# Performance work log

Measured on AMD Instinct MI355X. Metric: run time of the kernel, lower is better.

Reference implementation:

```python
import jax, jax.numpy as jnp
import numpy as np
from jax import lax

T_DATA = 20000
E_NO = 2000
I_NO = 500
SUB_NO = 16
SYN_B = 3
HID = 256
T_SYN = 200
T_ENC = 80


def _causal_conv(x, kern):
    # x: [T, S] per-subunit drive; kern: [S, K] causal kernels (index = lag)
    S, K = kern.shape
    lhs = jnp.pad(x.T, ((0, 0), (K - 1, 0)))[None]        # [1, S, T+K-1]
    rhs = kern[:, ::-1][:, None, :]                        # flip then correlate == torch conv1d path
    out = lax.conv_general_dilated(lhs, rhs, (1,), 'VALID', feature_group_count=S)
    return out[0].T                                        # [T, S]


def setup_inputs() -> dict:
    key = jax.random.key(0)
    ks = jax.random.split(key, 16)
    V_in = jax.random.normal(ks[0], (T_DATA,), jnp.float32) * 5.0 - 69.0
    S_e = jax.random.bernoulli(ks[1], 0.02, (T_DATA, E_NO)).astype(jnp.float32)
    S_i = jax.random.bernoulli(ks[2], 0.02, (T_DATA, I_NO)).astype(jnp.float32)
    # synapse -> subunit one-hot assignment matrices [sub_no, n_syn]
    C_syn_e = jax.nn.one_hot(jax.random.randint(ks[3], (E_NO,), 0, SUB_NO), SUB_NO, dtype=jnp.float32).T
    C_syn_i = jax.nn.one_hot(jax.random.randint(ks[4], (I_NO,), 0, SUB_NO), SUB_NO, dtype=jnp.float32).T
    # parameters, initialized exactly as in __init__
    K_syn = jnp.stack([jnp.full((SUB_NO, SYN_B), 0.04),
                       jnp.full((SUB_NO, SYN_B), -0.02),
                       jnp.full((SUB_NO, SYN_B), 0.02)], axis=-1)          # [sub, B, 3]
    tau_syn = jnp.tile((jnp.arange(SYN_B, dtype=jnp.float32) + 1.6)[:, None], (1, 3))  # [B, 3]
    delta_syn = jnp.full((SUB_NO, 2), 2.0, jnp.float32)
    enc_bias = jnp.zeros((SUB_NO - 1,), jnp.float32)
    W_in = 2 * T_ENC - 1

    def lin(k, fan_out, fan_in):
        kw, kb = jax.random.split(k)
        s = 1.0 / np.sqrt(fan_in)
        return (jax.random.uniform(kw, (fan_out, fan_in), jnp.float32, -s, s),
                jax.random.uniform(kb, (fan_out,), jnp.float32, -s, s))

    W1, b1 = lin(ks[5], HID, W_in)
    W2, b2 = lin(ks[6], HID, HID)
    W3, b3 = lin(ks[7], HID, HID)
    W4, b4 = lin(ks[8], SUB_NO - 1, HID)
    a1 = jnp.float32(0.25)
    a2 = jnp.float32(0.25)
    a3 = jnp.float32(0.25)
    return dict(V_in=V_in, S_e=S_e, S_i=S_i, C_syn_e=C_syn_e, C_syn_i=C_syn_i,
                K_syn=K_syn, tau_syn=tau_syn, delta_syn=delta_syn, enc_bias=enc_bias,
                W1=W1, b1=b1, a1=a1, W2=W2, b2=b2, a2=a2, W3=W3, b3=b3, a3=a3,
                W4=W4, b4=b4)


def reference(V_in, S_e, S_i, C_syn_e, C_syn_i, K_syn, tau_syn, delta_syn, enc_bias,
              W1, b1, a1, W2, b2, a2, W3, b3, a3, W4, b4):
    T = V_in.shape[0]
    # ---- spike_convolve, fully vectorized over (subunit, basis) ----
    t = jnp.arange(T_SYN, dtype=V_in.dtype)                 # [T_syn]
    d = jnp.exp(delta_syn)                                   # [sub, 2]
    te = jnp.maximum(t[None, :] - d[:, 0:1], 0.0)            # [sub, T_syn]
    ti = jnp.maximum(t[None, :] - d[:, 1:2], 0.0)
    tau = jnp.exp(tau_syn)                                   # [B, 3]
    tte = te[:, None, :] / tau[None, :, 0, None]             # [sub, B, T_syn]
    tti = ti[:, None, :] / tau[None, :, 1, None]
    ker_e = jnp.einsum('sbt,sb->st', tte * jnp.exp(-tte), K_syn[:, :, 0])
    ker_i = jnp.einsum('sbt,sb->st', tti * jnp.exp(-tti), K_syn[:, :, 1])
    in_e = S_e @ C_syn_e.T                                   # [T, sub]
    in_i = S_i @ C_syn_i.T
    S_conv = _causal_conv(in_e, ker_e) + _causal_conv(in_i, ker_i)   # [T, sub]
    # ---- encode: batched sliding-window MLP (replaces per-timestep loop) ----
    W = 2 * T_ENC - 1
    Vpad = jnp.zeros((T + W,), V_in.dtype).at[T_ENC - 1:T_ENC - 1 + T].set(V_in)
    idx = jnp.arange(T)[:, None] + jnp.arange(W)[None, :]    # [T, W]
    win = Vpad[idx]                                          # [T, W]
    prelu = lambda x, a: jnp.where(x >= 0, x, a * x)
    h = prelu(win @ W1.T + b1, a1)
    h = prelu(h @ W2.T + b2, a2)
    h = prelu(h @ W3.T + b3, a3)
    nn_out = h @ W4.T + b4                                   # [T, sub-1]
    return jax.nn.sigmoid(nn_out + S_conv[:, 1:] + enc_bias)
```

## Files before the change

kernel.cpp:

```cpp
#include <hip/hip_runtime.h>
#include <cstdint>
#include <cstddef>

#define T_DATA 20000
#define E_NO 2000
#define I_NO 500
#define SUB_NO 16
#define HID 256
#define T_SYN 200
#define T_ENC 80
#define W_IN 159

typedef __attribute__((ext_vector_type(8))) __bf16 bf16x8;
typedef __attribute__((ext_vector_type(8))) short short8;
typedef __attribute__((ext_vector_type(4))) float floatx4;
typedef __attribute__((ext_vector_type(4))) unsigned int uint4v;
typedef __attribute__((ext_vector_type(2))) unsigned int uint2v;

__device__ __forceinline__ float bf2f(unsigned short u) {
    union { unsigned int i; float f; } v; v.i = ((unsigned int)u) << 16; return v.f;
}
__device__ __forceinline__ unsigned short f2bf(float f) {
    union { float f; unsigned int i; } v; v.f = f;
    unsigned int r = v.i + 0x7FFFu + ((v.i >> 16) & 1u);
    return (unsigned short)(r >> 16);
}
__device__ __forceinline__ float inload(const void* p, int i, int isbf) {
    return isbf ? bf2f(((const unsigned short*)p)[i]) : ((const float*)p)[i];
}

__device__ __forceinline__ int detect_bf(const void* Se, int* sfl) {
    if (threadIdx.x == 0) *sfl = 0;
    __syncthreads();
    const unsigned int* w = (const unsigned int*)Se;
    int la = 0;
    #pragma unroll
    for (int i = 0; i < 4; i++)
        la |= (w[i * 256 + threadIdx.x] & 0xFFFFu) ? 1 : 0;
    if (la) atomicOr(sfl, 1);
    __syncthreads();
    return *sfl;
}

#define OFF_KERE   16u
#define OFF_KERI   12816u
#define OFF_SHE    25616u
#define OFF_SHI    33616u
#define OFF_W1H    35616u
#define OFF_W1L    117536u
#define OFF_W2H    199456u
#define OFF_W2L    330528u
#define OFF_W3H    461600u
#define OFF_W3L    592672u
#define OFF_W4H    723744u
#define OFF_W4L    731936u
#define OFF_INE    740128u
#define OFF_INI    1060128u

__global__ void k_tables(const void* Se, const void* Ksyn, const void* tau_syn, const void* dly,
                         const void* Ce, const void* Ci,
                         float* ker_e, float* ker_i, unsigned char* sh_e, unsigned char* sh_i) {
    __shared__ int sfl;
    int f = detect_bf(Se, &sfl);
    int id = blockIdx.x * 256 + threadIdx.x;
    if (id < 6400) {
        int c = id < 3200 ? 0 : 1;
        int q = id - c * 3200;
        int s = q / 200, j = q - s * 200;
        float d = expf(inload(dly, s * 2 + c, f));
        float tt = fmaxf((float)j - d, 0.0f);
        float acc = 0.f;
        #pragma unroll
        for (int b = 0; b < 3; b++) {
            float tau = expf(inload(tau_syn, b * 3 + c, f));
            float x = tt / tau;
            acc += x * expf(-x) * inload(Ksyn, (s * 3 + b) * 3 + c, f);
        }
        (c == 0 ? ker_e : ker_i)[s * 200 + j] = acc;
    } else if (id < 8400) {
        int e = id - 6400;
        int a = 0;
        for (int s = 0; s < 16; s++) if (inload(Ce, s * E_NO + e, f) > 0.5f) a = s;
        sh_e[e] = (unsigned char)(a * 8);
    } else if (id < 8900) {
        int e = id - 8400;
        int a = 0;
        for (int s = 0; s < 16; s++) if (inload(Ci, s * I_NO + e, f) > 0.5f) a = s;
        sh_i[e] = (unsigned char)(a * 8);
    }
}

__device__ __forceinline__ void acc_slot(unsigned int b, unsigned int sh,
                                         unsigned long long& lo, unsigned long long& hi) {
    unsigned int up = sh >> 6;
    unsigned int s6 = sh & 63;
    lo += (unsigned long long)(b & (up ^ 1u)) << s6;
    hi += (unsigned long long)(b & up) << s6;
}

__global__ void __launch_bounds__(256) k_spikes(const void* Se, const void* Si,
                         const unsigned char* sh_e, const unsigned char* sh_i,
                         const void* W1, const void* W2, const void* W3, const void* W4,
                         unsigned char* in_e, unsigned char* in_i,
                         unsigned short* W1h, unsigned short* W1l,
                         unsigned short* W2h, unsigned short* W2l,
                         unsigned short* W3h, unsigned short* W3l,
                         unsigned short* W4h, unsigned short* W4l) {
    __shared__ int sfl;
    __shared__ __align__(8) unsigned char she[E_NO];
    __shared__ __align__(8) unsigned char shi[I_NO];
    for (int i = threadIdx.x; i < E_NO / 4; i += 256)
        ((unsigned int*)she)[i] = ((const unsigned int*)sh_e)[i];
    for (int i = threadIdx.x; i < I_NO / 4; i += 256)
        ((unsigned int*)shi)[i] = ((const unsigned int*)sh_i)[i];
    int f = detect_bf(Se, &sfl);
    int lane = threadIdx.x & 63;
    int wave = threadIdx.x >> 6;
    int t = blockIdx.x * 4 + wave;
    unsigned long long e0 = 0, e1 = 0, i0 = 0, i1 = 0;
    if (f) {
        const uint4v* re = (const uint4v*)((const unsigned short*)Se + (size_t)t * E_NO);
        #pragma unroll
        for (int it = 0; it < 4; it++) {
            int c = it * 64 + lane;
            if (c < 250) {
                uint4v v = re[c];
                unsigned long long q = *(const unsigned long long*)&she[c * 8];
                #pragma unroll
                for (int w = 0; w < 4; w++) {
                    unsigned int x = v[w];
                    acc_slot((x >> 7) & 1u,  (unsigned int)(q >> (16 * w)) & 0xFFu, e0, e1);
                    acc_slot((x >> 23) & 1u, (unsigned int)(q >> (16 * w + 8)) & 0xFFu, e0, e1);
                }
            }
        }
        const uint2v* ri = (const uint2v*)((const unsigned short*)Si + (size_t)t * I_NO);
        #pragma unroll
        for (int it = 0; it < 2; it++) {
            int c = it * 64 + lane;
            if (c < 125) {
                uint2v v = ri[c];
                unsigned int q = *(const unsigned int*)&shi[c * 4];
                #pragma unroll
                for (int w = 0; w < 2; w++) {
                    unsigned int x = v[w];
                    acc_slot((x >> 7) & 1u,  (q >> (16 * w)) & 0xFFu, i0, i1);
                    acc_slot((x >> 23) & 1u, (q >> (16 * w + 8)) & 0xFFu, i0, i1);
                }
            }
        }
    } else {
        const uint4v* re = (const uint4v*)((const float*)Se + (size_t)t * E_NO);
        #pragma unroll
        for (int it = 0; it < 8; it++) {
            int c = it * 64 + lane;
            if (c < 500) {
                uint4v v = re[c];
                unsigned int q = *(const unsigned int*)&she[c * 4];
                #pragma unroll
                for (int w = 0; w < 4; w++)
                    acc_slot((v[w] >> 23) & 1u, (q >> (8 * w)) & 0xFFu, e0, e1);
            }
        }
        const uint2v* ri = (const uint2v*)((const float*)Si + (size_t)t * I_NO);
        #pragma unroll
        for (int it = 0; it < 4; it++) {
            int c = it * 64 + lane;
            if (c < 250) {
                uint2v v = ri[c];
                unsigned int q = *(const unsigned short*)&shi[c * 2];
                #pragma unroll
                for (int w = 0; w < 2; w++)
                    acc_slot((v[w] >> 23) & 1u, (q >> (8 * w)) & 0xFFu, i0, i1);
            }
        }
    }
    for (int off = 32; off; off >>= 1) {
        e0 += __shfl_xor(e0, off);
        e1 += __shfl_xor(e1, off);
        i0 += __shfl_xor(i0, off);
        i1 += __shfl_xor(i1, off);
    }
    if (lane < 16) {
        unsigned long long a = (lane < 8) ? e0 : e1;
        in_e[(size_t)t * 16 + lane] = (unsigned char)((a >> ((lane & 7) * 8)) & 0xFF);
    } else if (lane < 32) {
        int s = lane - 16;
        unsigned long long a = (s < 8) ? i0 : i1;
        in_i[(size_t)t * 16 + s] = (unsigned char)((a >> ((s & 7) * 8)) & 0xFF);
    }
    if (blockIdx.x < 688) {
        int q = blockIdx.x * 256 + threadIdx.x;
        if (q < 40960) {
            int j = q & 7, l = (q >> 3) & 63, r = q >> 9;
            int ks = r % 5, tile = r / 5;
            int n = tile * 16 + (l & 15);
            int k = ks * 32 + (l >> 4) * 8 + j;
            float v = (k < W_IN) ? inload(W1, n * W_IN + k, f) : 0.f;
            unsigned short hi = f2bf(v);
            W1h[q] = hi;
            W1l[q] = f2bf(v - bf2f(hi));
        } else if (q < 106496) {
            int p = q - 40960;
            int j = p & 7, l = (p >> 3) & 63, r = p >> 9;
            int ks = r & 7, tile = r >> 3;
            int n = tile * 16 + (l & 15);
            int k = ks * 32 + (l >> 4) * 8 + j;
            float v = inload(W2, n * 256 + k, f);
            unsigned short hi = f2bf(v);
            W2h[p] = hi;
            W2l[p] = f2bf(v - bf2f(hi));
        } else if (q < 172032) {
            int p = q - 106496;
            int j = p & 7, l = (p >> 3) & 63, r = p >> 9;
            int ks = r & 7, tile = r >> 3;
            int n = tile * 16 + (l & 15);
            int k = ks * 32 + (l >> 4) * 8 + j;
            float v = inload(W3, n * 256 + k, f);
            unsigned short hi = f2bf(v);
            W3h[p] = hi;
            W3l[p] = f2bf(v - bf2f(hi));
        } else {
            int p = q - 172032;
            int j = p & 7, l = (p >> 3) & 63, ks = p >> 9;
            int lm = l & 15, quad = l >> 4;
            float v = 0.f;
            if (lm < 15) v = inload(W4, lm * 256 + ks * 32 + quad * 8 + j, f);
            unsigned short hi = f2bf(v);
            W4h[p] = hi;
            W4l[p] = f2bf(v - bf2f(hi));
        }
    }
}

template<bool BF>
__device__ __forceinline__ void mlp_body(
    const void* V,
    const unsigned short* W1h, const unsigned short* W1l, const void* b1, const void* a1p,
    const unsigned short* W2h, const unsigned short* W2l, const void* b2, const void* a2p,
    const unsigned short* W3h, const unsigned short* W3l, const void* b3, const void* a3p,
    const unsigned short* W4h, const unsigned short* W4l, const void* b4,
    const void* encb, const float* Sc, void* out,
    unsigned short* Ahi, unsigned short* Alo,
    const bf16x8 (&Bh1)[5][4])
{
    int tid = threadIdx.x;
    int lane = tid & 63, wave = tid >> 6;
    int lm = lane & 15, quad = lane >> 4;
    int t0 = blockIdx.x * 64;

    auto ld = [&](const void* p, int i) -> float {
        return BF ? bf2f(((const unsigned short*)p)[i]) : ((const float*)p)[i];
    };
    auto boff1 = [&](int ks, int nt) { return (size_t)((((wave * 4 + nt) * 5 + ks) * 64 + lane) << 3); };
    auto boff  = [&](int ks, int nt) { return (size_t)((((wave * 4 + nt) * 8 + ks) * 64 + lane) << 3); };

    for (int idx = tid; idx < 64 * 160; idx += 256) {
        int m = idx / 160, k = idx - m * 160;
        int tg = t0 + m + k - (T_ENC - 1);
        float v = 0.f;
        if (k < W_IN && tg >= 0 && tg < T_DATA) v = ld(V, tg);
        unsigned short hi = f2bf(v);
        int col = (((k >> 3) ^ (m & 31)) << 3) | (k & 7);
        Ahi[m * 256 + col] = hi;
        if (!BF) Alo[m * 256 + col] = f2bf(v - bf2f(hi));
    }
    __syncthreads();

    floatx4 acc[4][4];
    auto aoff = [&](int mt, int ks) {
        int arow = mt * 16 + lm;
        return arow * 256 + ((((ks << 2) | quad) ^ (arow & 31)) << 3);
    };

    auto epi = [&](const void* bias, float alpha) {
        __syncthreads();
        #pragma unroll
        for (int mt = 0; mt < 4; mt++) {
            #pragma unroll
            for (int nt = 0; nt < 4; nt++) {
                int cn = wave * 64 + nt * 16 + lm;
                float bb = ld(bias, cn);
                #pragma unroll
                for (int j = 0; j < 4; j++) {
                    int row = mt * 16 + quad * 4 + j;
                    float h = acc[mt][nt][j] + bb;
                    h = (h >= 0.f) ? h : alpha * h;
                    unsigned short hi = f2bf(h);
                    int col = (((cn >> 3) ^ (row & 31)) << 3) | (cn & 7);
                    Ahi[row * 256 + col] = hi;
                    if (!BF) Alo[row * 256 + col] = f2bf(h - bf2f(hi));
                }
            }
        }
        __syncthreads();
    };

    floatx4 z = {0.f, 0.f, 0.f, 0.f};
    {
        #pragma unroll
        for (int mt = 0; mt < 4; mt++)
            #pragma unroll
            for (int nt = 0; nt < 4; nt++) acc[mt][nt] = z;
        if (BF) {
            #pragma unroll
            for (int ks = 0; ks < 5; ks++) {
                bf16x8 a[4];
                #pragma unroll
                for (int mt = 0; mt < 4; mt++) a[mt] = *(const bf16x8*)&Ahi[aoff(mt, ks)];
                #pragma unroll
                for (int nt = 0; nt < 4; nt++)
                    #pragma unroll
                    for (int mt = 0; mt < 4; mt++)
                        acc[mt][nt] = __builtin_amdgcn_mfma_f32_16x16x32_bf16(a[mt], Bh1[ks][nt], acc[mt][nt], 0, 0, 0);
            }
        } else {
            #pragma unroll
            for (int ks = 0; ks < 5; ks++) {
                bf16x8 ah[4], al[4];
                #pragma unroll
                for (int mt = 0; mt < 4; mt++) {
                    ah[mt] = *(const bf16x8*)&Ahi[aoff(mt, ks)];
                    al[mt] = *(const bf16x8*)&Alo[aoff(mt, ks)];
                }
                #pragma unroll
                for (int nt = 0; nt < 4; nt++) {
                    bf16x8 bh = Bh1[ks][nt];
                    bf16x8 bl = *(const bf16x8*)(W1l + boff1(ks, nt));
                    #pragma unroll
                    for (int mt = 0; mt < 4; mt++) {
                        acc[mt][nt] = __builtin_amdgcn_mfma_f32_16x16x32_bf16(ah[mt], bh, acc[mt][nt], 0, 0, 0);
                        acc[mt][nt] = __builtin_amdgcn_mfma_f32_16x16x32_bf16(al[mt], bh, acc[mt][nt], 0, 0, 0);
                        acc[mt][nt] = __builtin_amdgcn_mfma_f32_16x16x32_bf16(ah[mt], bl, acc[mt][nt], 0, 0, 0);
                    }
                }
            }
        }
        epi(b1, ld(a1p, 0));
    }
    const unsigned short* Whs[2] = {W2h, W3h};
    const unsigned short* Wls[2] = {W2l, W3l};
    const void* bs[2] = {b2, b3};
    const void* as_[2] = {a2p, a3p};
    for (int l = 0; l < 2; l++) {
        #pragma unroll
        for (int mt = 0; mt < 4; mt++)
            #pragma unroll
            for (int nt = 0; nt < 4; nt++) acc[mt][nt] = z;
        const unsigned short* Wh = Whs[l];
        const unsigned short* Wl = Wls[l];
        if (BF) {
            bf16x8 Bh[8][4];
            #pragma unroll
            for (int ks = 0; ks < 8; ks++)
                #pragma unroll
                for (int nt = 0; nt < 4; nt++)
                    Bh[ks][nt] = *(const bf16x8*)(Wh + boff(ks, nt));
            #pragma unroll
            for (int ks = 0; ks < 8; ks++) {
                bf16x8 a[4];
                #pragma unroll
                for (int mt = 0; mt < 4; mt++) a[mt] = *(const bf16x8*)&Ahi[aoff(mt, ks)];
                #pragma unroll
                for (int nt = 0; nt < 4; nt++)
                    #pragma unroll
                    for (int mt = 0; mt < 4; mt++)
                        acc[mt][nt] = __builtin_amdgcn_mfma_f32_16x16x32_bf16(a[mt], Bh[ks][nt], acc[mt][nt], 0, 0, 0);
            }
        } else {
            #pragma unroll
            for (int ks = 0; ks < 8; ks++) {
                bf16x8 ah[4], al[4];
                #pragma unroll
                for (int mt = 0; mt < 4; mt++) {
                    ah[mt] = *(const bf16x8*)&Ahi[aoff(mt, ks)];
                    al[mt] = *(const bf16x8*)&Alo[aoff(mt, ks)];
                }
                #pragma unroll
                for (int nt = 0; nt < 4; nt++) {
                    bf16x8 bh = *(const bf16x8*)(Wh + boff(ks, nt));
                    bf16x8 bl = *(const bf16x8*)(Wl + boff(ks, nt));
                    #pragma unroll
                    for (int mt = 0; mt < 4; mt++) {
                        acc[mt][nt] = __builtin_amdgcn_mfma_f32_16x16x32_bf16(ah[mt], bh, acc[mt][nt], 0, 0, 0);
                        acc[mt][nt] = __builtin_amdgcn_mfma_f32_16x16x32_bf16(al[mt], bh, acc[mt][nt], 0, 0, 0);
                        acc[mt][nt] = __builtin_amdgcn_mfma_f32_16x16x32_bf16(ah[mt], bl, acc[mt][nt], 0, 0, 0);
                    }
                }
            }
        }
        epi(bs[l], ld(as_[l], 0));
    }
    {
        int mt = wave;
        floatx4 a4 = z;
        #pragma unroll
        for (int ks = 0; ks < 8; ks++) {
            bf16x8 ah = *(const bf16x8*)&Ahi[aoff(mt, ks)];
            bf16x8 bh = *(const bf16x8*)(W4h + (size_t)((ks * 64 + lane) << 3));
            a4 = __builtin_amdgcn_mfma_f32_16x16x32_bf16(ah, bh, a4, 0, 0, 0);
            if (!BF) {
                bf16x8 al = *(const bf16x8*)&Alo[aoff(mt, ks)];
                bf16x8 bl = *(const bf16x8*)(W4l + (size_t)((ks * 64 + lane) << 3));
                a4 = __builtin_amdgcn_mfma_f32_16x16x32_bf16(al, bh, a4, 0, 0, 0);
                a4 = __builtin_amdgcn_mfma_f32_16x16x32_bf16(ah, bl, a4, 0, 0, 0);
            }
        }
        if (lm < 15) {
            float bb = ld(b4, lm) + ld(encb, lm);
            #pragma unroll
            for (int j = 0; j < 4; j++) {
                int row = mt * 16 + quad * 4 + j;
                int t = t0 + row;
                if (t < T_DATA) {
                    float x = a4[j] + bb + Sc[row * 16 + lm + 1];
                    x = fminf(fmaxf(x, -40.f), 40.f);
                    float sg = 1.f / (1.f + expf(-x));
                    if (BF) ((unsigned short*)out)[(size_t)t * 15 + lm] = f2bf(sg);
                    else    ((float*)out)[(size_t)t * 15 + lm] = sg;
                }
            }
        }
    }
}

__global__ void __launch_bounds__(256, 2) k_convmlp(
    const void* Se, const void* V,
    const unsigned char* in_e, const unsigned char* in_i,
    const float* ker_e, const float* ker_i,
    const unsigned short* W1h, const unsigned short* W1l, const void* b1, const void* a1p,
    const unsigned short* W2h, const unsigned short* W2l, const void* b2, const void* a2p,
    const unsigned short* W3h, const unsigned short* W3l, const void* b3, const void* a3p,
    const unsigned short* W4h, const unsigned short* W4l, const void* b4,
    const void* encb, void* out) {
    __shared__ __align__(16) unsigned char smem[65536];
    __shared__ __align__(16) float Sc[64 * 16];
    __shared__ int sfl;

    float* se = (float*)smem;
    float* si = se + 263 * 17;
    float* ke = si + 263 * 17;
    float* ki = ke + 16 * 201;

    int lane = threadIdx.x & 63, wave = threadIdx.x >> 6;

    bf16x8 Bh1[5][4];
    #pragma unroll
    for (int ks = 0; ks < 5; ks++)
        #pragma unroll
        for (int nt = 0; nt < 4; nt++)
            Bh1[ks][nt] = *(const bf16x8*)(W1h + (size_t)((((wave * 4 + nt) * 5 + ks) * 64 + lane) << 3));

    int t0 = blockIdx.x * 64;
    for (int idx = threadIdx.x; idx < 263 * 4; idx += 256) {
        int r = idx >> 2, wi = idx & 3;
        int t = t0 - 199 + r;
        unsigned int ve = 0, vi = 0;
        if (t >= 0 && t < T_DATA) {
            ve = ((const unsigned int*)in_e)[t * 4 + wi];
            vi = ((const unsigned int*)in_i)[t * 4 + wi];
        }
        #pragma unroll
        for (int b = 0; b < 4; b++) {
            se[r * 17 + wi * 4 + b] = (float)((ve >> (8 * b)) & 0xFF);
            si[r * 17 + wi * 4 + b] = (float)((vi >> (8 * b)) & 0xFF);
        }
    }
    for (int idx = threadIdx.x; idx < 3200; idx += 256) {
        int s2 = idx / 200, j = idx - s2 * 200;
        ke[s2 * 201 + j] = ker_e[idx];
        ki[s2 * 201 + j] = ker_i[idx];
    }
    int f = detect_bf(Se, &sfl);

    {
        int s = threadIdx.x & 15, g4 = (threadIdx.x >> 4) * 4;
        float a0 = 0.f, a1 = 0.f, a2 = 0.f, a3 = 0.f;
        float w0 = se[(g4 + 199) * 17 + s], w1 = se[(g4 + 200) * 17 + s];
        float w2 = se[(g4 + 201) * 17 + s], w3 = se[(g4 + 202) * 17 + s];
        float x0 = si[(g4 + 199) * 17 + s], x1 = si[(g4 + 200) * 17 + s];
        float x2 = si[(g4 + 201) * 17 + s], x3 = si[(g4 + 202) * 17 + s];
        #pragma unroll 4
        for (int j = 0; j < 200; j++) {
            float kej = ke[s * 201 + j];
            float kij = ki[s * 201 + j];
            a0 += w0 * kej + x0 * kij;
            a1 += w1 * kej + x1 * kij;
            a2 += w2 * kej + x2 * kij;
            a3 += w3 * kej + x3 * kij;
            int lr = g4 + 198 - j; lr = lr < 0 ? 0 : lr;
            float nw = se[lr * 17 + s], nx = si[lr * 17 + s];
            w3 = w2; w2 = w1; w1 = w0; w0 = nw;
            x3 = x2; x2 = x1; x1 = x0; x0 = nx;
        }
        Sc[(g4 + 0) * 16 + s] = a0;
        Sc[(g4 + 1) * 16 + s] = a1;
        Sc[(g4 + 2) * 16 + s] = a2;
        Sc[(g4 + 3) * 16 + s] = a3;
    }
    __syncthreads();

    unsigned short* Ahi = (unsigned short*)smem;
    unsigned short* Alo = Ahi + 64 * 256;
    if (f)
        mlp_body<true>(V, W1h, W1l, b1, a1p, W2h, W2l, b2, a2p, W3h, W3l, b3, a3p,
                       W4h, W4l, b4, encb, Sc, out, Ahi, Alo, Bh1);
    else
        mlp_body<false>(V, W1h, W1l, b1, a1p, W2h, W2l, b2, a2p, W3h, W3l, b3, a3p,
                        W4h, W4l, b4, encb, Sc, out, Ahi, Alo, Bh1);
}

extern "C" void kernel_launch(void* const* d_in, const int* in_sizes, int n_in,
                              void* d_out, int out_size, void* d_ws, size_t ws_size,
                              hipStream_t stream) {
    const void* V    = d_in[0];
    const void* Se   = d_in[1];
    const void* Si   = d_in[2];
    const void* Ce   = d_in[3];
    const void* Ci   = d_in[4];
    const void* Ksyn = d_in[5];
    const void* tau  = d_in[6];
    const void* dly  = d_in[7];
    const void* encb = d_in[8];
    const void* W1   = d_in[9];
    const void* b1   = d_in[10];
    const void* a1   = d_in[11];
    const void* W2   = d_in[12];
    const void* b2   = d_in[13];
    const void* a2   = d_in[14];
    const void* W3   = d_in[15];
    const void* b3   = d_in[16];
    const void* a3   = d_in[17];
    const void* W4   = d_in[18];
    const void* b4   = d_in[19];

    char* w = (char*)d_ws;
    float* ker_e = (float*)(w + OFF_KERE);
    float* ker_i = (float*)(w + OFF_KERI);
    unsigned char* sh_e = (unsigned char*)(w + OFF_SHE);
    unsigned char* sh_i = (unsigned char*)(w + OFF_SHI);
    unsigned short* W1h = (unsigned short*)(w + OFF_W1H);
    unsigned short* W1l = (unsigned short*)(w + OFF_W1L);
    unsigned short* W2h = (unsigned short*)(w + OFF_W2H);
    unsigned short* W2l = (unsigned short*)(w + OFF_W2L);
    unsigned short* W3h = (unsigned short*)(w + OFF_W3H);
    unsigned short* W3l = (unsigned short*)(w + OFF_W3L);
    unsigned short* W4h = (unsigned short*)(w + OFF_W4H);
    unsigned short* W4l = (unsigned short*)(w + OFF_W4L);
    unsigned char* in_e = (unsigned char*)(w + OFF_INE);
    unsigned char* in_i = (unsigned char*)(w + OFF_INI);

    k_tables<<<35, 256, 0, stream>>>(Se, Ksyn, tau, dly, Ce, Ci,
                                     ker_e, ker_i, sh_e, sh_i);
    k_spikes<<<5000, 256, 0, stream>>>(Se, Si, sh_e, sh_i, W1, W2, W3, W4,
                                       in_e, in_i,
                                       W1h, W1l, W2h, W2l, W3h, W3l, W4h, W4l);
    k_convmlp<<<313, 256, 0, stream>>>(Se, V, in_e, in_i, ker_e, ker_i,
                                       W1h, W1l, b1, a1, W2h, W2l, b2, a2,
                                       W3h, W3l, b3, a3, W4h, W4l, b4,
                                       encb, d_out);
}
```

Before: 355.4 us.

## Use 512-thread blocks in conv+MLP kernel, split N tiles across 8 waves

Doubles the block size of the fused conv/MLP kernel to 512 threads. Each wave now covers two N tiles instead of four, and the first half of the threads runs the causal convolution while the second half builds the sliding-window input tile. The spike and kernel tables in shared memory are stored in bf16/padded form, and the fp32 low-part activations move to a global workspace. The aim is more waves per block to hide latency and to overlap conv with input staging. In exchange, low-part accesses on the fp32 path now go to global memory, and the final layer uses only half of the waves.

```diff
diff --git a/kernel.cpp b/kernel.cpp
--- a/kernel.cpp
+++ b/kernel.cpp
@@ -29,14 +29,15 @@
     return isbf ? bf2f(((const unsigned short*)p)[i]) : ((const float*)p)[i];
 }
 
+template<int BLK>
 __device__ __forceinline__ int detect_bf(const void* Se, int* sfl) {
     if (threadIdx.x == 0) *sfl = 0;
     __syncthreads();
     const unsigned int* w = (const unsigned int*)Se;
     int la = 0;
     #pragma unroll
-    for (int i = 0; i < 4; i++)
-        la |= (w[i * 256 + threadIdx.x] & 0xFFFFu) ? 1 : 0;
+    for (int i = 0; i < 1024 / BLK; i++)
+        la |= (w[i * BLK + threadIdx.x] & 0xFFFFu) ? 1 : 0;
     if (la) atomicOr(sfl, 1);
     __syncthreads();
     return *sfl;
@@ -56,12 +57,13 @@
 #define OFF_W4L    731936u
 #define OFF_INE    740128u
 #define OFF_INI    1060128u
+#define OFF_ALO    1380128u
 
 __global__ void k_tables(const void* Se, const void* Ksyn, const void* tau_syn, const void* dly,
                          const void* Ce, const void* Ci,
                          float* ker_e, float* ker_i, unsigned char* sh_e, unsigned char* sh_i) {
     __shared__ int sfl;
-    int f = detect_bf(Se, &sfl);
+    int f = detect_bf<256>(Se, &sfl);
     int id = blockIdx.x * 256 + threadIdx.x;
     if (id < 6400) {
         int c = id < 3200 ? 0 : 1;
@@ -113,7 +115,7 @@
         ((unsigned int*)she)[i] = ((const unsigned int*)sh_e)[i];
     for (int i = threadIdx.x; i < I_NO / 4; i += 256)
         ((unsigned int*)shi)[i] = ((const unsigned int*)sh_i)[i];
-    int f = detect_bf(Se, &sfl);
+    int f = detect_bf<256>(Se, &sfl);
     int lane = threadIdx.x & 63;
     int wave = threadIdx.x >> 6;
     int t = blockIdx.x * 4 + wave;
@@ -235,14 +237,13 @@
 
 template<bool BF>
 __device__ __forceinline__ void mlp_body(
-    const void* V,
-    const unsigned short* W1h, const unsigned short* W1l, const void* b1, const void* a1p,
+    const unsigned short* W1l, const void* b1, const void* a1p,
     const unsigned short* W2h, const unsigned short* W2l, const void* b2, const void* a2p,
     const unsigned short* W3h, const unsigned short* W3l, const void* b3, const void* a3p,
     const unsigned short* W4h, const unsigned short* W4l, const void* b4,
     const void* encb, const float* Sc, void* out,
-    unsigned short* Ahi, unsigned short* Alo,
-    const bf16x8 (&Bh1)[5][4])
+    unsigned short* Ahi, unsigned short* AloG,
+    const bf16x8 (&Bh1)[5][2])
 {
     int tid = threadIdx.x;
     int lane = tid & 63, wave = tid >> 6;
@@ -252,86 +253,74 @@
     auto ld = [&](const void* p, int i) -> float {
         return BF ? bf2f(((const unsigned short*)p)[i]) : ((const float*)p)[i];
     };
-    auto boff1 = [&](int ks, int nt) { return (size_t)((((wave * 4 + nt) * 5 + ks) * 64 + lane) << 3); };
-    auto boff  = [&](int ks, int nt) { return (size_t)((((wave * 4 + nt) * 8 + ks) * 64 + lane) << 3); };
-
-    for (int idx = tid; idx < 64 * 160; idx += 256) {
-        int m = idx / 160, k = idx - m * 160;
-        int tg = t0 + m + k - (T_ENC - 1);
-        float v = 0.f;
-        if (k < W_IN && tg >= 0 && tg < T_DATA) v = ld(V, tg);
-        unsigned short hi = f2bf(v);
-        int col = (((k >> 3) ^ (m & 31)) << 3) | (k & 7);
-        Ahi[m * 256 + col] = hi;
-        if (!BF) Alo[m * 256 + col] = f2bf(v - bf2f(hi));
-    }
-    __syncthreads();
-
-    floatx4 acc[4][4];
+    auto boff1 = [&](int ks, int ntl) {
+        int tile = wave * 2 + ntl;
+        return (size_t)(((tile * 5 + ks) * 64 + lane) << 3);
+    };
+    auto boff = [&](int ks, int ntl) {
+        int tile = wave * 2 + ntl;
+        return (size_t)(((tile * 8 + ks) * 64 + lane) << 3);
+    };
     auto aoff = [&](int mt, int ks) {
         int arow = mt * 16 + lm;
         return arow * 256 + ((((ks << 2) | quad) ^ (arow & 31)) << 3);
     };
 
+    floatx4 z = {0.f, 0.f, 0.f, 0.f};
+    floatx4 acc[4][2];
+
     auto epi = [&](const void* bias, float alpha) {
         __syncthreads();
         #pragma unroll
         for (int mt = 0; mt < 4; mt++) {
             #pragma unroll
-            for (int nt = 0; nt < 4; nt++) {
-                int cn = wave * 64 + nt * 16 + lm;
+            for (int ntl = 0; ntl < 2; ntl++) {
+                int cn = (wave * 2 + ntl) * 16 + lm;
                 float bb = ld(bias, cn);
                 #pragma unroll
                 for (int j = 0; j < 4; j++) {
                     int row = mt * 16 + quad * 4 + j;
-                    float h = acc[mt][nt][j] + bb;
+                    float h = acc[mt][ntl][j] + bb;
                     h = (h >= 0.f) ? h : alpha * h;
                     unsigned short hi = f2bf(h);
                     int col = (((cn >> 3) ^ (row & 31)) << 3) | (cn & 7);
                     Ahi[row * 256 + col] = hi;
-                    if (!BF) Alo[row * 256 + col] = f2bf(h - bf2f(hi));
+                    if (!BF) AloG[row * 256 + col] = f2bf(h - bf2f(hi));
                 }
             }
         }
         __syncthreads();
     };
 
-    floatx4 z = {0.f, 0.f, 0.f, 0.f};
     {
         #pragma unroll
         for (int mt = 0; mt < 4; mt++)
             #pragma unroll
-            for (int nt = 0; nt < 4; nt++) acc[mt][nt] = z;
-        if (BF) {
-            #pragma unroll
-            for (int ks = 0; ks < 5; ks++) {
-                bf16x8 a[4];
-                #pragma unroll
-                for (int mt = 0; mt < 4; mt++) a[mt] = *(const bf16x8*)&Ahi[aoff(mt, ks)];
-                #pragma unroll
-                for (int nt = 0; nt < 4; nt++)
+            for (int ntl = 0; ntl < 2; ntl++) acc[mt][ntl] = z;
+        #pragma unroll
+        for (int ks = 0; ks < 5; ks++) {
+            bf16x8 ah[4];
+            #pragma unroll
+            for (int mt = 0; mt < 4; mt++) ah[mt] = *(const bf16x8*)&Ahi[aoff(mt, ks)];
+            if (BF) {
+                #pragma unroll
+                for (int ntl = 0; ntl < 2; ntl++)
                     #pragma unroll
                     for (int mt = 0; mt < 4; mt++)
-                        acc[mt][nt] = __builtin_amdgcn_mfma_f32_16x16x32_bf16(a[mt], Bh1[ks][nt], acc[mt][nt], 0, 0, 0);
-            }
-        } else {
-            #pragma unroll
-            for (int ks = 0; ks < 5; ks++) {
-                bf16x8 ah[4], al[4];
-                #pragma unroll
-                for (int mt = 0; mt < 4; mt++) {
-                    ah[mt] = *(const bf16x8*)&Ahi[aoff(mt, ks)];
-                    al[mt] = *(const bf16x8*)&Alo[aoff(mt, ks)];
-                }
-                #pragma unroll
-                for (int nt = 0; nt < 4; nt++) {
-                    bf16x8 bh = Bh1[ks][nt];
-                    bf16x8 bl = *(const bf16x8*)(W1l + boff1(ks, nt));
+                        acc[mt][ntl] = __builtin_amdgcn_mfma_f32_16x16x32_bf16(ah[mt], Bh1[ks][ntl], acc[mt][ntl], 0, 0, 0);
+            } else {
+                bf16x8 al[4];
+                #pragma unroll
+                for (int mt = 0; mt < 4; mt++) al[mt] = *(const bf16x8*)(AloG + aoff(mt, ks));
+                #pragma unroll
+                for (int ntl = 0; ntl < 2; ntl++) {
+                    bf16x8 bh = Bh1[ks][ntl];
+                    bf16x8 bl = *(const bf16x8*)(W1l + boff1(ks, ntl));
                     #pragma unroll
                     for (int mt = 0; mt < 4; mt++) {
-                        acc[mt][nt] = __builtin_amdgcn_mfma_f32_16x16x32_bf16(ah[mt], bh, acc[mt][nt], 0, 0, 0);
-                        acc[mt][nt] = __builtin_amdgcn_mfma_f32_16x16x32_bf16(al[mt], bh, acc[mt][nt], 0, 0, 0);
-                        acc[mt][nt] = __builtin_amdgcn_mfma_f32_16x16x32_bf16(ah[mt], bl, acc[mt][nt], 0, 0, 0);
+                        acc[mt][ntl] = __builtin_amdgcn_mfma_f32_16x16x32_bf16(ah[mt], bh, acc[mt][ntl], 0, 0, 0);
+                        acc[mt][ntl] = __builtin_amdgcn_mfma_f32_16x16x32_bf16(al[mt], bh, acc[mt][ntl], 0, 0, 0);
+                        acc[mt][ntl] = __builtin_amdgcn_mfma_f32_16x16x32_bf16(ah[mt], bl, acc[mt][ntl], 0, 0, 0);
                     }
                 }
             }
@@ -346,52 +335,49 @@
         #pragma unroll
         for (int mt = 0; mt < 4; mt++)
             #pragma unroll
-            for (int nt = 0; nt < 4; nt++) acc[mt][nt] = z;
+            for (int ntl = 0; ntl < 2; ntl++) acc[mt][ntl] = z;
         const unsigned short* Wh = Whs[l];
         const unsigned short* Wl = Wls[l];
-        if (BF) {
-            bf16x8 Bh[8][4];
-            #pragma unroll
-            for (int ks = 0; ks < 8; ks++)
-                #pragma unroll
-                for (int nt = 0; nt < 4; nt++)
-                    Bh[ks][nt] = *(const bf16x8*)(Wh + boff(ks, nt));
-            #pragma unroll
-            for (int ks = 0; ks < 8; ks++) {
-                bf16x8 a[4];
-                #pragma unroll
-                for (int mt = 0; mt < 4; mt++) a[mt] = *(const bf16x8*)&Ahi[aoff(mt, ks)];
-                #pragma unroll
-                for (int nt = 0; nt < 4; nt++)
+        #pragma unroll
+        for (int half = 0; half < 2; half++) {
+            bf16x8 Bh[4][2];
+            #pragma unroll
+            for (int c = 0; c < 4; c++)
+                #pragma unroll
+                for (int ntl = 0; ntl < 2; ntl++)
+                    Bh[c][ntl] = *(const bf16x8*)(Wh + boff(half * 4 + c, ntl));
+            #pragma unroll
+            for (int c = 0; c < 4; c++) {
+                int ks = half * 4 + c;
+                bf16x8 ah[4];
+                #pragma unroll
+                for (int mt = 0; mt < 4; mt++) ah[mt] = *(const bf16x8*)&Ahi[aoff(mt, ks)];
+                if (BF) {
                     #pragma unroll
-                    for (int mt = 0; mt < 4; mt++)
-                        acc[mt][nt] = __builtin_amdgcn_mfma_f32_16x16x32_bf16(a[mt], Bh[ks][nt], acc[mt][nt], 0, 0, 0);
-            }
-        } else {
-            #pragma unroll
-            for (int ks = 0; ks < 8; ks++) {
-                bf16x8 ah[4], al[4];
-                #pragma unroll
-                for (int mt = 0; mt < 4; mt++) {
-                    ah[mt] = *(const bf16x8*)&Ahi[aoff(mt, ks)];
-                    al[mt] = *(const bf16x8*)&Alo[aoff(mt, ks)];
-                }
-                #pragma unroll
-                for (int nt = 0; nt < 4; nt++) {
-                    bf16x8 bh = *(const bf16x8*)(Wh + boff(ks, nt));
-                    bf16x8 bl = *(const bf16x8*)(Wl + boff(ks, nt));
+                    for (int ntl = 0; ntl < 2; ntl++)
+                        #pragma unroll
+                        for (int mt = 0; mt < 4; mt++)
+                            acc[mt][ntl] = __builtin_amdgcn_mfma_f32_16x16x32_bf16(ah[mt], Bh[c][ntl], acc[mt][ntl], 0, 0, 0);
+                } else {
+                    bf16x8 al[4];
                     #pragma unroll
-                    for (int mt = 0; mt < 4; mt++) {
-                        acc[mt][nt] = __builtin_amdgcn_mfma_f32_16x16x32_bf16(ah[mt], bh, acc[mt][nt], 0, 0, 0);
-                        acc[mt][nt] = __builtin_amdgcn_mfma_f32_16x16x32_bf16(al[mt], bh, acc[mt][nt], 0, 0, 0);
-                        acc[mt][nt] = __builtin_amdgcn_mfma_f32_16x16x32_bf16(ah[mt], bl, acc[mt][nt], 0, 0, 0);
+                    for (int mt = 0; mt < 4; mt++) al[mt] = *(const bf16x8*)(AloG + aoff(mt, ks));
+                    #pragma unroll
+                    for (int ntl = 0; ntl < 2; ntl++) {
+                        bf16x8 bl = *(const bf16x8*)(Wl + boff(ks, ntl));
+                        #pragma unroll
+                        for (int mt = 0; mt < 4; mt++) {
+                            acc[mt][ntl] = __builtin_amdgcn_mfma_f32_16x16x32_bf16(ah[mt], Bh[c][ntl], acc[mt][ntl], 0, 0, 0);
+                            acc[mt][ntl] = __builtin_amdgcn_mfma_f32_16x16x32_bf16(al[mt], Bh[c][ntl], acc[mt][ntl], 0, 0, 0);
+                            acc[mt][ntl] = __builtin_amdgcn_mfma_f32_16x16x32_bf16(ah[mt], bl, acc[mt][ntl], 0, 0, 0);
+                        }
                     }
                 }
             }
         }
         epi(bs[l], ld(as_[l], 0));
     }
-    {
+    if (wave < 4) {
         int mt = wave;
         floatx4 a4 = z;
         #pragma unroll
@@ -400,7 +386,7 @@
             bf16x8 bh = *(const bf16x8*)(W4h + (size_t)((ks * 64 + lane) << 3));
             a4 = __builtin_amdgcn_mfma_f32_16x16x32_bf16(ah, bh, a4, 0, 0, 0);
             if (!BF) {
-                bf16x8 al = *(const bf16x8*)&Alo[aoff(mt, ks)];
+                bf16x8 al = *(const bf16x8*)(AloG + aoff(mt, ks));
                 bf16x8 bl = *(const bf16x8*)(W4l + (size_t)((ks * 64 + lane) << 3));
                 a4 = __builtin_amdgcn_mfma_f32_16x16x32_bf16(al, bh, a4, 0, 0, 0);
                 a4 = __builtin_amdgcn_mfma_f32_16x16x32_bf16(ah, bl, a4, 0, 0, 0);
@@ -424,7 +410,7 @@
     }
 }
 
-__global__ void __launch_bounds__(256, 2) k_convmlp(
+__global__ void __launch_bounds__(512, 4) k_convmlp(
     const void* Se, const void* V,
     const unsigned char* in_e, const unsigned char* in_i,
     const float* ker_e, const float* ker_i,
@@ -432,27 +418,28 @@
     const unsigned short* W2h, const unsigned short* W2l, const void* b2, const void* a2p,
     const unsigned short* W3h, const unsigned short* W3l, const void* b3, const void* a3p,
     const unsigned short* W4h, const unsigned short* W4l, const void* b4,
-    const void* encb, void* out) {
-    __shared__ __align__(16) unsigned char smem[65536];
+    const void* encb, unsigned short* AloBase, void* out) {
+    __shared__ __align__(16) unsigned short se16[263 * 17];
+    __shared__ __align__(16) unsigned short si16[263 * 17];
+    __shared__ __align__(16) float kef[16 * 204];
+    __shared__ __align__(16) float kif[16 * 204];
+    __shared__ __align__(16) unsigned short Ahi[64 * 256];
     __shared__ __align__(16) float Sc[64 * 16];
     __shared__ int sfl;
 
-    float* se = (float*)smem;
-    float* si = se + 263 * 17;
-    float* ke = si + 263 * 17;
-    float* ki = ke + 16 * 201;
-
-    int lane = threadIdx.x & 63, wave = threadIdx.x >> 6;
-
-    bf16x8 Bh1[5][4];
+    int tid = threadIdx.x;
+    int lane = tid & 63, wave = tid >> 6;
+    int t0 = blockIdx.x * 64;
+    unsigned short* AloG = AloBase + (size_t)blockIdx.x * 64 * 256;
+
+    bf16x8 Bh1[5][2];
     #pragma unroll
     for (int ks = 0; ks < 5; ks++)
         #pragma unroll
-        for (int nt = 0; nt < 4; nt++)
-            Bh1[ks][nt] = *(const bf16x8*)(W1h + (size_t)((((wave * 4 + nt) * 5 + ks) * 64 + lane) << 3));
-
-    int t0 = blockIdx.x * 64;
-    for (int idx = threadIdx.x; idx < 263 * 4; idx += 256) {
+        for (int ntl = 0; ntl < 2; ntl++)
+            Bh1[ks][ntl] = *(const bf16x8*)(W1h + (size_t)((((wave * 2 + ntl) * 5 + ks) * 64 + lane) << 3));
+
+    for (int idx = tid; idx < 263 * 4; idx += 512) {
         int r = idx >> 2, wi = idx & 3;
         int t = t0 - 199 + r;
         unsigned int ve = 0, vi = 0;
@@ -462,52 +449,64 @@
         }
         #pragma unroll
         for (int b = 0; b < 4; b++) {
-            se[r * 17 + wi * 4 + b] = (float)((ve >> (8 * b)) & 0xFF);
-            si[r * 17 + wi * 4 + b] = (float)((vi >> (8 * b)) & 0xFF);
-        }
-    }
-    for (int idx = threadIdx.x; idx < 3200; idx += 256) {
+            se16[r * 17 + wi * 4 + b] = f2bf((float)((ve >> (8 * b)) & 0xFF));
+            si16[r * 17 + wi * 4 + b] = f2bf((float)((vi >> (8 * b)) & 0xFF));
+        }
+    }
+    for (int idx = tid; idx < 3200; idx += 512) {
         int s2 = idx / 200, j = idx - s2 * 200;
-        ke[s2 * 201 + j] = ker_e[idx];
-        ki[s2 * 201 + j] = ker_i[idx];
-    }
-    int f = detect_bf(Se, &sfl);
-
-    {
-        int s = threadIdx.x & 15, g4 = (threadIdx.x >> 4) * 4;
+        kef[s2 * 204 + j] = ker_e[idx];
+        kif[s2 * 204 + j] = ker_i[idx];
+    }
+    int f = detect_bf<512>(Se, &sfl);
+
+    if (tid < 256) {
+        int s = tid & 15, g4 = (tid >> 4) * 4;
         float a0 = 0.f, a1 = 0.f, a2 = 0.f, a3 = 0.f;
-        float w0 = se[(g4 + 199) * 17 + s], w1 = se[(g4 + 200) * 17 + s];
-        float w2 = se[(g4 + 201) * 17 + s], w3 = se[(g4 + 202) * 17 + s];
-        float x0 = si[(g4 + 199) * 17 + s], x1 = si[(g4 + 200) * 17 + s];
-        float x2 = si[(g4 + 201) * 17 + s], x3 = si[(g4 + 202) * 17 + s];
-        #pragma unroll 4
-        for (int j = 0; j < 200; j++) {
-            float kej = ke[s * 201 + j];
-            float kij = ki[s * 201 + j];
-            a0 += w0 * kej + x0 * kij;
-            a1 += w1 * kej + x1 * kij;
-            a2 += w2 * kej + x2 * kij;
-            a3 += w3 * kej + x3 * kij;
-            int lr = g4 + 198 - j; lr = lr < 0 ? 0 : lr;
-            float nw = se[lr * 17 + s], nx = si[lr * 17 + s];
-            w3 = w2; w2 = w1; w1 = w0; w0 = nw;
-            x3 = x2; x2 = x1; x1 = x0; x0 = nx;
+        float w0 = bf2f(se16[(g4 + 199) * 17 + s]), w1 = bf2f(se16[(g4 + 200) * 17 + s]);
+        float w2 = bf2f(se16[(g4 + 201) * 17 + s]), w3 = bf2f(se16[(g4 + 202) * 17 + s]);
+        float x0 = bf2f(si16[(g4 + 199) * 17 + s]), x1 = bf2f(si16[(g4 + 200) * 17 + s]);
+        float x2 = bf2f(si16[(g4 + 201) * 17 + s]), x3 = bf2f(si16[(g4 + 202) * 17 + s]);
+        for (int j = 0; j < 200; j += 4) {
+            floatx4 ke4 = *(const floatx4*)&kef[s * 204 + j];
+            floatx4 ki4 = *(const floatx4*)&kif[s * 204 + j];
+            #pragma unroll
+            for (int q = 0; q < 4; q++) {
+                float kej = ke4[q], kij = ki4[q];
+                a0 += w0 * kej + x0 * kij;
+                a1 += w1 * kej + x1 * kij;
+                a2 += w2 * kej + x2 * kij;
+                a3 += w3 * kej + x3 * kij;
+                int lr = g4 + 198 - j - q; lr = lr < 0 ? 0 : lr;
+                float nw = bf2f(se16[lr * 17 + s]), nx = bf2f(si16[lr * 17 + s]);
+                w3 = w2; w2 = w1; w1 = w0; w0 = nw;
+                x3 = x2; x2 = x1; x1 = x0; x0 = nx;
+            }
         }
         Sc[(g4 + 0) * 16 + s] = a0;
         Sc[(g4 + 1) * 16 + s] = a1;
         Sc[(g4 + 2) * 16 + s] = a2;
         Sc[(g4 + 3) * 16 + s] = a3;
+    } else {
+        for (int idx = tid - 256; idx < 64 * 160; idx += 256) {
+            int m = idx / 160, k = idx - m * 160;
+            int tg = t0 + m + k - (T_ENC - 1);
+            float v = 0.f;
+            if (k < W_IN && tg >= 0 && tg < T_DATA) v = inload(V, tg, f);
+            unsigned short hi = f2bf(v);
+            int col = (((k >> 3) ^ (m & 31)) << 3) | (k & 7);
+            Ahi[m * 256 + col] = hi;
+            if (!f) AloG[m * 256 + col] = f2bf(v - bf2f(hi));
+        }
     }
     __syncthreads();
 
-    unsigned short* Ahi = (unsigned short*)smem;
-    unsigned short* Alo = Ahi + 64 * 256;
     if (f)
-        mlp_body<true>(V, W1h, W1l, b1, a1p, W2h, W2l, b2, a2p, W3h, W3l, b3, a3p,
-                       W4h, W4l, b4, encb, Sc, out, Ahi, Alo, Bh1);
+        mlp_body<true>(W1l, b1, a1p, W2h, W2l, b2, a2p, W3h, W3l, b3, a3p,
+                       W4h, W4l, b4, encb, Sc, out, Ahi, AloG, Bh1);
     else
-        mlp_body<false>(V, W1h, W1l, b1, a1p, W2h, W2l, b2, a2p, W3h, W3l, b3, a3p,
-                        W4h, W4l, b4, encb, Sc, out, Ahi, Alo, Bh1);
+        mlp_body<false>(W1l, b1, a1p, W2h, W2l, b2, a2p, W3h, W3l, b3, a3p,
+                        W4h, W4l, b4, encb, Sc, out, Ahi, AloG, Bh1);
 }
 
 extern "C" void kernel_launch(void* const* d_in, const int* in_sizes, int n_in,
@@ -549,14 +548,15 @@
     unsigned short* W4l = (unsigned short*)(w + OFF_W4L);
     unsigned char* in_e = (unsigned char*)(w + OFF_INE);
     unsigned char* in_i = (unsigned char*)(w + OFF_INI);
+    unsigned short* AloB = (unsigned short*)(w + OFF_ALO);
 
     k_tables<<<35, 256, 0, stream>>>(Se, Ksyn, tau, dly, Ce, Ci,
                                      ker_e, ker_i, sh_e, sh_i);
     k_spikes<<<5000, 256, 0, stream>>>(Se, Si, sh_e, sh_i, W1, W2, W3, W4,
                                        in_e, in_i,
                                        W1h, W1l, W2h, W2l, W3h, W3l, W4h, W4l);
-    k_convmlp<<<313, 256, 0, stream>>>(Se, V, in_e, in_i, ker_e, ker_i,
+    k_convmlp<<<313, 512, 0, stream>>>(Se, V, in_e, in_i, ker_e, ker_i,
                                        W1h, W1l, b1, a1, W2h, W2l, b2, a2,
                                        W3h, W3l, b3, a3, W4h, W4l, b4,
-                                       encb, d_out);
-}
+                                       encb, AloB, d_out);
+}
```

New measurement: 448.1 us. +26.1%, slower.

## Software-pipeline weight fragment loads across MLP layers in bf16 path

Applied to the files above, without the earlier changes.

In the bf16 path, the MLP layer chain is unrolled and W2/W3/W4 weight fragments are loaded in half-K chunks into double registers (Bc/Bn). Each chunk is issued before the previous layer's epilogue or the other half's MFMAs, so global load latency overlaps with compute and barriers. This replaces the earlier pattern of loading all 32 fragments of a layer up front after the epilogue. Register pressure stays similar (two 16-fragment buffers instead of one 32-fragment buffer) but could still affect occupancy under launch_bounds(256,2).

```diff
diff --git a/kernel.cpp b/kernel.cpp
--- a/kernel.cpp
+++ b/kernel.cpp
@@ -297,24 +297,135 @@
     };
 
     floatx4 z = {0.f, 0.f, 0.f, 0.f};
-    {
+
+    if (BF) {
+        bf16x8 Bc[4][4], Bn[4][4];
         #pragma unroll
         for (int mt = 0; mt < 4; mt++)
             #pragma unroll
             for (int nt = 0; nt < 4; nt++) acc[mt][nt] = z;
-        if (BF) {
-            #pragma unroll
-            for (int ks = 0; ks < 5; ks++) {
-                bf16x8 a[4];
-                #pragma unroll
-                for (int mt = 0; mt < 4; mt++) a[mt] = *(const bf16x8*)&Ahi[aoff(mt, ks)];
-                #pragma unroll
-                for (int nt = 0; nt < 4; nt++)
-                    #pragma unroll
-                    for (int mt = 0; mt < 4; mt++)
-                        acc[mt][nt] = __builtin_amdgcn_mfma_f32_16x16x32_bf16(a[mt], Bh1[ks][nt], acc[mt][nt], 0, 0, 0);
-            }
-        } else {
+        #pragma unroll
+        for (int ks = 0; ks < 5; ks++) {
+            bf16x8 a[4];
+            #pragma unroll
+            for (int mt = 0; mt < 4; mt++) a[mt] = *(const bf16x8*)&Ahi[aoff(mt, ks)];
+            #pragma unroll
+            for (int nt = 0; nt < 4; nt++)
+                #pragma unroll
+                for (int mt = 0; mt < 4; mt++)
+                    acc[mt][nt] = __builtin_amdgcn_mfma_f32_16x16x32_bf16(a[mt], Bh1[ks][nt], acc[mt][nt], 0, 0, 0);
+        }
+        #pragma unroll
+        for (int c = 0; c < 4; c++)
+            #pragma unroll
+            for (int nt = 0; nt < 4; nt++)
+                Bc[c][nt] = *(const bf16x8*)(W2h + boff(c, nt));
+        epi(b1, ld(a1p, 0));
+
+        #pragma unroll
+        for (int mt = 0; mt < 4; mt++)
+            #pragma unroll
+            for (int nt = 0; nt < 4; nt++) acc[mt][nt] = z;
+        #pragma unroll
+        for (int c = 0; c < 4; c++)
+            #pragma unroll
+            for (int nt = 0; nt < 4; nt++)
+                Bn[c][nt] = *(const bf16x8*)(W2h + boff(4 + c, nt));
+        #pragma unroll
+        for (int c = 0; c < 4; c++) {
+            bf16x8 a[4];
+            #pragma unroll
+            for (int mt = 0; mt < 4; mt++) a[mt] = *(const bf16x8*)&Ahi[aoff(mt, c)];
+            #pragma unroll
+            for (int nt = 0; nt < 4; nt++)
+                #pragma unroll
+                for (int mt = 0; mt < 4; mt++)
+                    acc[mt][nt] = __builtin_amdgcn_mfma_f32_16x16x32_bf16(a[mt], Bc[c][nt], acc[mt][nt], 0, 0, 0);
+        }
+        #pragma unroll
+        for (int c = 0; c < 4; c++)
+            #pragma unroll
+            for (int nt = 0; nt < 4; nt++)
+                Bc[c][nt] = *(const bf16x8*)(W3h + boff(c, nt));
+        #pragma unroll
+        for (int c = 0; c < 4; c++) {
+            bf16x8 a[4];
+            #pragma unroll
+            for (int mt = 0; mt < 4; mt++) a[mt] = *(const bf16x8*)&Ahi[aoff(mt, 4 + c)];
+            #pragma unroll
+            for (int nt = 0; nt < 4; nt++)
+                #pragma unroll
+                for (int mt = 0; mt < 4; mt++)
+                    acc[mt][nt] = __builtin_amdgcn_mfma_f32_16x16x32_bf16(a[mt], Bn[c][nt], acc[mt][nt], 0, 0, 0);
+        }
+        epi(b2, ld(a2p, 0));
+
+        #pragma unroll
+        for (int mt = 0; mt < 4; mt++)
+            #pragma unroll
+            for (int nt = 0; nt < 4; nt++) acc[mt][nt] = z;
+        #pragma unroll
+        for (int c = 0; c < 4; c++)
+            #pragma unroll
+            for (int nt = 0; nt < 4; nt++)
+                Bn[c][nt] = *(const bf16x8*)(W3h + boff(4 + c, nt));
+        #pragma unroll
+        for (int c = 0; c < 4; c++) {
+            bf16x8 a[4];
+            #pragma unroll
+            for (int mt = 0; mt < 4; mt++) a[mt] = *(const bf16x8*)&Ahi[aoff(mt, c)];
+            #pragma unroll
+            for (int nt = 0; nt < 4; nt++)
+                #pragma unroll
+                for (int mt = 0; mt < 4; mt++)
+                    acc[mt][nt] = __builtin_amdgcn_mfma_f32_16x16x32_bf16(a[mt], Bc[c][nt], acc[mt][nt], 0, 0, 0);
+        }
+        bf16x8 w4[8];
+        #pragma unroll
+        for (int ks = 0; ks < 8; ks++)
+            w4[ks] = *(const bf16x8*)(W4h + (size_t)((ks * 64 + lane) << 3));
+        #pragma unroll
+        for (int c = 0; c < 4; c++) {
+            bf16x8 a[4];
+            #pragma unroll
+            for (int mt = 0; mt < 4; mt++) a[mt] = *(const bf16x8*)&Ahi[aoff(mt, 4 + c)];
+            #pragma unroll
+            for (int nt = 0; nt < 4; nt++)
+                #pragma unroll
+                for (int mt = 0; mt < 4; mt++)
+                    acc[mt][nt] = __builtin_amdgcn_mfma_f32_16x16x32_bf16(a[mt], Bn[c][nt], acc[mt][nt], 0, 0, 0);
+        }
+        epi(b3, ld(a3p, 0));
+
+        {
+            int mt = wave;
+            floatx4 a4 = z;
+            #pragma unroll
+            for (int ks = 0; ks < 8; ks++) {
+                bf16x8 ah = *(const bf16x8*)&Ahi[aoff(mt, ks)];
+                a4 = __builtin_amdgcn_mfma_f32_16x16x32_bf16(ah, w4[ks], a4, 0, 0, 0);
+            }
+            if (lm < 15) {
+                float bb = ld(b4, lm) + ld(encb, lm);
+                #pragma unroll
+                for (int j = 0; j < 4; j++) {
+                    int row = mt * 16 + quad * 4 + j;
+                    int t = t0 + row;
+                    if (t < T_DATA) {
+                        float x = a4[j] + bb + Sc[row * 16 + lm + 1];
+                        x = fminf(fmaxf(x, -40.f), 40.f);
+                        float sg = 1.f / (1.f + expf(-x));
+                        ((unsigned short*)out)[(size_t)t * 15 + lm] = f2bf(sg);
+                    }
+                }
+            }
+        }
+    } else {
+        {
+            #pragma unroll
+            for (int mt = 0; mt < 4; mt++)
+                #pragma unroll
+                for (int nt = 0; nt < 4; nt++) acc[mt][nt] = z;
             #pragma unroll
             for (int ks = 0; ks < 5; ks++) {
                 bf16x8 ah[4], al[4];
@@ -335,39 +446,19 @@
                     }
                 }
             }
-        }
-        epi(b1, ld(a1p, 0));
-    }
-    const unsigned short* Whs[2] = {W2h, W3h};
-    const unsigned short* Wls[2] = {W2l, W3l};
-    const void* bs[2] = {b2, b3};
-    const void* as_[2] = {a2p, a3p};
-    for (int l = 0; l < 2; l++) {
-        #pragma unroll
-        for (int mt = 0; mt < 4; mt++)
-            #pragma unroll
-            for (int nt = 0; nt < 4; nt++) acc[mt][nt] = z;
-        const unsigned short* Wh = Whs[l];
-        const unsigned short* Wl = Wls[l];
-        if (BF) {
-            bf16x8 Bh[8][4];
-            #pragma unroll
-            for (int ks = 0; ks < 8; ks++)
-                #pragma unroll
-                for (int nt = 0; nt < 4; nt++)
-                    Bh[ks][nt] = *(const bf16x8*)(Wh + boff(ks, nt));
-            #pragma unroll
-            for (int ks = 0; ks < 8; ks++) {
-                bf16x8 a[4];
-                #pragma unroll
-                for (int mt = 0; mt < 4; mt++) a[mt] = *(const bf16x8*)&Ahi[aoff(mt, ks)];
-                #pragma unroll
-                for (int nt = 0; nt < 4; nt++)
-                    #pragma unroll
-                    for (int mt = 0; mt < 4; mt++)
-                        acc[mt][nt] = __builtin_amdgcn_mfma_f32_16x16x32_bf16(a[mt], Bh[ks][nt], acc[mt][nt], 0, 0, 0);
-            }
-        } else {
+            epi(b1, ld(a1p, 0));
+        }
+        const unsigned short* Whs[2] = {W2h, W3h};
+        const unsigned short* Wls[2] = {W2l, W3l};
+        const void* bs[2] = {b2, b3};
+        const void* as_[2] = {a2p, a3p};
+        for (int l = 0; l < 2; l++) {
+            #pragma unroll
+            for (int mt = 0; mt < 4; mt++)
+                #pragma unroll
+                for (int nt = 0; nt < 4; nt++) acc[mt][nt] = z;
+            const unsigned short* Wh = Whs[l];
+            const unsigned short* Wl = Wls[l];
             #pragma unroll
             for (int ks = 0; ks < 8; ks++) {
                 bf16x8 ah[4], al[4];
@@ -388,36 +479,33 @@
                     }
                 }
             }
-        }
-        epi(bs[l], ld(as_[l], 0));
-    }
-    {
-        int mt = wave;
-        floatx4 a4 = z;
-        #pragma unroll
-        for (int ks = 0; ks < 8; ks++) {
-            bf16x8 ah = *(const bf16x8*)&Ahi[aoff(mt, ks)];
-            bf16x8 bh = *(const bf16x8*)(W4h + (size_t)((ks * 64 + lane) << 3));
-            a4 = __builtin_amdgcn_mfma_f32_16x16x32_bf16(ah, bh, a4, 0, 0, 0);
-            if (!BF) {
+            epi(bs[l], ld(as_[l], 0));
+        }
+        {
+            int mt = wave;
+            floatx4 a4 = z;
+            #pragma unroll
+            for (int ks = 0; ks < 8; ks++) {
+                bf16x8 ah = *(const bf16x8*)&Ahi[aoff(mt, ks)];
+                bf16x8 bh = *(const bf16x8*)(W4h + (size_t)((ks * 64 + lane) << 3));
+                a4 = __builtin_amdgcn_mfma_f32_16x16x32_bf16(ah, bh, a4, 0, 0, 0);
                 bf16x8 al = *(const bf16x8*)&Alo[aoff(mt, ks)];
                 bf16x8 bl = *(const bf16x8*)(W4l + (size_t)((ks * 64 + lane) << 3));
                 a4 = __builtin_amdgcn_mfma_f32_16x16x32_bf16(al, bh, a4, 0, 0, 0);
                 a4 = __builtin_amdgcn_mfma_f32_16x16x32_bf16(ah, bl, a4, 0, 0, 0);
             }
-        }
-        if (lm < 15) {
-            float bb = ld(b4, lm) + ld(encb, lm);
-            #pragma unroll
-            for (int j = 0; j < 4; j++) {
-                int row = mt * 16 + quad * 4 + j;
-                int t = t0 + row;
-                if (t < T_DATA) {
-                    float x = a4[j] + bb + Sc[row * 16 + lm + 1];
-                    x = fminf(fmaxf(x, -40.f), 40.f);
-                    float sg = 1.f / (1.f + expf(-x));
-                    if (BF) ((unsigned short*)out)[(size_t)t * 15 + lm] = f2bf(sg);
-                    else    ((float*)out)[(size_t)t * 15 + lm] = sg;
+            if (lm < 15) {
+                float bb = ld(b4, lm) + ld(encb, lm);
+                #pragma unroll
+                for (int j = 0; j < 4; j++) {
+                    int row = mt * 16 + quad * 4 + j;
+                    int t = t0 + row;
+                    if (t < T_DATA) {
+                        float x = a4[j] + bb + Sc[row * 16 + lm + 1];
+                        x = fminf(fmaxf(x, -40.f), 40.f);
+                        float sg = 1.f / (1.f + expf(-x));
+                        ((float*)out)[(size_t)t * 15 + lm] = sg;
+                    }
                 }
             }
         }
```

New measurement: 356.6 us. No clear change (+0.4%).
